# Optimization experiments

Hardware: AMD Instinct MI355X
Metric: run time of the kernel (lower is better)

The kernel has to match this reference:

```python
import jax, jax.numpy as jnp
import numpy as np

B, N, F_IN, D_OUT, EMB_DIM = 4, 2048, 64, 128, 16
H1, D1 = 4, D_OUT // 4   # gat1: 4 heads, 32 per head
H2, D2 = 1, D_OUT        # gat2: 1 head, 128
NEG_INF = -1e9
LN_EPS = 1e-3  # keras LayerNormalization default epsilon


def setup_inputs() -> dict:
    key = jax.random.key(0)
    ks = jax.random.split(key, 12)
    def glorot(k, shape):
        lim = np.sqrt(6.0 / (shape[0] + shape[1]))
        return jax.random.uniform(k, shape, jnp.float32, -lim, lim)
    return {
        "x": jax.random.normal(ks[0], (B, N, F_IN), jnp.float32),
        "emb": glorot(ks[1], (N, EMB_DIM)),
        "q1_w": glorot(ks[2], (F_IN, H1 * D1)), "q1_b": jnp.zeros((H1 * D1,), jnp.float32),
        "k1_w": glorot(ks[3], (F_IN, H1 * D1)), "k1_b": jnp.zeros((H1 * D1,), jnp.float32),
        "v1_w": glorot(ks[4], (F_IN, H1 * D1)), "v1_b": jnp.zeros((H1 * D1,), jnp.float32),
        "q2_w": glorot(ks[5], (D_OUT, H2 * D2)), "q2_b": jnp.zeros((H2 * D2,), jnp.float32),
        "k2_w": glorot(ks[6], (D_OUT, H2 * D2)), "k2_b": jnp.zeros((H2 * D2,), jnp.float32),
        "v2_w": glorot(ks[7], (D_OUT, H2 * D2)), "v2_b": jnp.zeros((H2 * D2,), jnp.float32),
        "proj_w": glorot(ks[8], (F_IN, D_OUT)),
        "ln_g": jnp.ones((D_OUT,), jnp.float32),
        "ln_b": jnp.zeros((D_OUT,), jnp.float32),
    }


def _adaptive_adj(emb):
    # tf.math.l2_normalize(axis=-1, epsilon=1e-12)
    sq = jnp.maximum(jnp.sum(emb * emb, axis=-1, keepdims=True), 1e-12)
    n = emb * jax.lax.rsqrt(sq)
    adj = jax.nn.sigmoid(n @ n.T)
    eye = jnp.eye(N, dtype=jnp.float32)
    return adj + eye - adj * eye  # force diag to 1


def _graph_attention(x, adj, qw, qb, kw, kb, vw, vb, heads, d):
    b, n, _ = x.shape
    q = (x @ qw + qb).reshape(b, n, heads, d)
    k = (x @ kw + kb).reshape(b, n, heads, d)
    v = (x @ vw + vb).reshape(b, n, heads, d)
    scores = jnp.einsum('bihd,bjhd->bhij', q, k) / jnp.sqrt(jnp.float32(d))
    scores = jnp.where(adj[None, None] == 0, NEG_INF, scores)
    w = jax.nn.softmax(scores, axis=-1)  # dropout inactive (training=False)
    out = jnp.einsum('bhij,bjhd->bihd', w, v)
    return out.reshape(b, n, heads * d)


def reference(x, emb, q1_w, q1_b, k1_w, k1_b, v1_w, v1_b,
              q2_w, q2_b, k2_w, k2_b, v2_w, v2_b, proj_w, ln_g, ln_b):
    input_projected = x @ proj_w
    adj = _adaptive_adj(emb)
    h = _graph_attention(x, adj, q1_w, q1_b, k1_w, k1_b, v1_w, v1_b, H1, D1)
    h = jax.nn.relu(h)
    h = _graph_attention(h, adj, q2_w, q2_b, k2_w, k2_b, v2_w, v2_b, H2, D2)
    y = h + input_projected
    mu = jnp.mean(y, axis=-1, keepdims=True)
    var = jnp.mean((y - mu) ** 2, axis=-1, keepdims=True)
    return (y - mu) * jax.lax.rsqrt(var + LN_EPS) * ln_g + ln_b
```

## Files before the change

### kernel.cpp

```cpp
#include <hip/hip_runtime.h>
#include <hip/hip_bf16.h>

#define NB 4
#define NN 2048
#define FIN 64
#define DOUT 128

typedef __hip_bfloat16 bf16;
typedef __attribute__((ext_vector_type(8))) short short8;
typedef __attribute__((ext_vector_type(4))) float f32x4;
typedef __attribute__((ext_vector_type(4))) int int4v;

static __device__ __forceinline__ float bf2f(bf16 v) { return __bfloat162float(v); }
static __device__ __forceinline__ bf16  f2bf(float v) { return __float2bfloat16(v); }
static __device__ __forceinline__ unsigned bfbits(float v) {
    bf16 h = __float2bfloat16(v);
    return (unsigned)*reinterpret_cast<unsigned short*>(&h);
}

#define VT_IDX(b, key, d) ((((size_t)(b)*32 + ((key) >> 6))*128 + (d))*64 + ((key) & 63))

__global__ __launch_bounds__(256) void k_gemm1(
    const float* __restrict__ x,
    const float* __restrict__ q1w, const float* __restrict__ q1b,
    const float* __restrict__ k1w, const float* __restrict__ k1b,
    const float* __restrict__ v1w, const float* __restrict__ v1b,
    const float* __restrict__ pw,
    bf16* __restrict__ qA, bf16* __restrict__ kA, bf16* __restrict__ vT,
    float* __restrict__ proj)
{
    __shared__ float At[64][65];
    __shared__ float Wt[64][65];
    const int rb = blockIdx.x;
    const int cb = blockIdx.y;
    const int mat = cb >> 1;
    const int c0 = (cb & 1) * 64;
    const float* W    = (mat==0)? q1w : (mat==1)? k1w : (mat==2)? v1w : pw;
    const float* bias = (mat==0)? q1b : (mat==1)? k1b : (mat==2)? v1b : nullptr;
    const int t = threadIdx.x;
    const int row0 = rb * 64;
    for (int e = t; e < 64*64; e += 256) {
        int r = e >> 6, c = e & 63;
        At[r][c] = x[(size_t)(row0 + r)*FIN + c];
        Wt[r][c] = W[r*DOUT + c0 + c];
    }
    __syncthreads();
    const int ty = t >> 4, tx = t & 15;
    float acc[4][4] = {};
    #pragma unroll 8
    for (int k = 0; k < 64; ++k) {
        float av[4], bv[4];
        #pragma unroll
        for (int i = 0; i < 4; ++i) av[i] = At[ty*4+i][k];
        #pragma unroll
        for (int j = 0; j < 4; ++j) bv[j] = Wt[k][tx*4+j];
        #pragma unroll
        for (int i = 0; i < 4; ++i)
            #pragma unroll
            for (int j = 0; j < 4; ++j)
                acc[i][j] = fmaf(av[i], bv[j], acc[i][j]);
    }
    #pragma unroll
    for (int i = 0; i < 4; ++i) {
        int gr = row0 + ty*4 + i;
        #pragma unroll
        for (int j = 0; j < 4; ++j) {
            int gc = c0 + tx*4 + j;
            float v = acc[i][j] + (bias ? bias[gc] : 0.f);
            if (mat == 0)      qA[(size_t)gr*DOUT + gc] = f2bf(v);
            else if (mat == 1) kA[(size_t)gr*DOUT + gc] = f2bf(v);
            else if (mat == 2) {
                int b = gr >> 11, n = gr & 2047;
                vT[VT_IDX(b, n, gc)] = f2bf(v);
            } else proj[(size_t)gr*DOUT + gc] = v;
        }
    }
}

__global__ __launch_bounds__(256) void k_gemm2(
    const bf16* __restrict__ h,
    const float* __restrict__ q2w, const float* __restrict__ q2b,
    const float* __restrict__ k2w, const float* __restrict__ k2b,
    const float* __restrict__ v2w, const float* __restrict__ v2b,
    bf16* __restrict__ qA, bf16* __restrict__ kA, bf16* __restrict__ vT)
{
    __shared__ float At[64][65];
    __shared__ float Wt[64][65];
    const int rb = blockIdx.x, cb = blockIdx.y;
    const int mat = cb >> 1, c0 = (cb & 1)*64;
    const float* W    = (mat==0)? q2w : (mat==1)? k2w : v2w;
    const float* bias = (mat==0)? q2b : (mat==1)? k2b : v2b;
    const int t = threadIdx.x, ty = t >> 4, tx = t & 15, row0 = rb*64;
    float acc[4][4] = {};
    for (int kc = 0; kc < 2; ++kc) {
        __syncthreads();
        for (int e = t; e < 64*64; e += 256) {
            int r = e >> 6, c = e & 63;
            At[r][c] = bf2f(h[(size_t)(row0+r)*DOUT + kc*64 + c]);
            Wt[r][c] = W[(kc*64+r)*DOUT + c0 + c];
        }
        __syncthreads();
        #pragma unroll 8
        for (int k = 0; k < 64; ++k) {
            float av[4], bv[4];
            #pragma unroll
            for (int i = 0; i < 4; ++i) av[i] = At[ty*4+i][k];
            #pragma unroll
            for (int j = 0; j < 4; ++j) bv[j] = Wt[k][tx*4+j];
            #pragma unroll
            for (int i = 0; i < 4; ++i)
                #pragma unroll
                for (int j = 0; j < 4; ++j)
                    acc[i][j] = fmaf(av[i], bv[j], acc[i][j]);
        }
    }
    #pragma unroll
    for (int i = 0; i < 4; ++i) {
        int gr = row0 + ty*4 + i;
        #pragma unroll
        for (int j = 0; j < 4; ++j) {
            int gc = c0 + tx*4 + j;
            float v = acc[i][j] + bias[gc];
            if (mat == 0)      qA[(size_t)gr*DOUT + gc] = f2bf(v);
            else if (mat == 1) kA[(size_t)gr*DOUT + gc] = f2bf(v);
            else {
                int b = gr >> 11, n = gr & 2047;
                vT[VT_IDX(b, n, gc)] = f2bf(v);
            }
        }
    }
}

template<int D, int MODE, int NW, int NQ>
__global__ __launch_bounds__(NW*64, 2) void k_attn_mfma(
    const bf16* __restrict__ qA, const bf16* __restrict__ kA, const bf16* __restrict__ vT,
    const float* __restrict__ proj, const float* __restrict__ lng, const float* __restrict__ lnb,
    bf16* __restrict__ hout, float* __restrict__ fout)
{
    constexpr int NKS = D / 32;
    constexpr int NMT = D / 16;
    constexpr int ITERS = NN / (64 * NW);

    __shared__ float lbuf[NW][NQ*16];
    constexpr int OSW = (MODE == 0) ? (D + 1) : (D + 2);
    __shared__ char oS_raw[(size_t)NW * NQ*16 * OSW * ((MODE == 0) ? 4 : 2)];

    const float scale = (D == 32) ? 0.17677669529663687f : 0.08838834764831843f;

    const unsigned wg  = blockIdx.x + (unsigned)gridDim.x * blockIdx.y;
    const unsigned xcd = wg & 7u;
    const unsigned idx = wg >> 3;
    int qb, bh;
    if constexpr (MODE == 0) {
        bh = (int)((xcd << 1) | (idx >> 5));
        qb = (int)(idx & 31u);
    } else {
        bh = (int)(xcd >> 1);
        qb = (int)(((xcd & 1u) << 5) | idx);
    }

    const int b  = (MODE == 0) ? (bh >> 2) : bh;
    const int hd = (MODE == 0) ? (bh & 3) : 0;
    const int q0 = qb * (16*NQ);
    const int wave = threadIdx.x >> 6, lane = threadIdx.x & 63;
    const int n16 = lane & 15, q4 = lane >> 4;

    const short* qbase = (const short*)qA + ((size_t)b*NN)*DOUT + hd*32;
    const short* kbase = (const short*)kA + ((size_t)b*NN)*DOUT + hd*32;
    const short* vbase = (const short*)vT + (size_t)b*32*128*64 + (size_t)(hd*32)*64;

    short8 qf[NQ][NKS];
    #pragma unroll
    for (int qq = 0; qq < NQ; ++qq)
        #pragma unroll
        for (int ks = 0; ks < NKS; ++ks)
            qf[qq][ks] = *(const short8*)(qbase + (size_t)(q0 + qq*16 + n16)*DOUT + ks*32 + q4*8);

    f32x4 acc[NQ][NMT];
    #pragma unroll
    for (int qq = 0; qq < NQ; ++qq)
        #pragma unroll
        for (int mt = 0; mt < NMT; ++mt) acc[qq][mt] = f32x4{0.f, 0.f, 0.f, 0.f};
    float l_lane[NQ];
    #pragma unroll
    for (int qq = 0; qq < NQ; ++qq) l_lane[qq] = 0.f;

    const int srcA = n16 + ((q4 & 1) * 2) * 16;
    const int srcB = srcA + 16;
    const bool selhi = (q4 >= 2);

    for (int kt0 = 0; kt0 < ITERS; ++kt0) {
        const int kt = wave * ITERS + kt0;
        const short* krow = kbase + (size_t)(kt*64)*DOUT;
        const short* vrow = vbase + (size_t)kt*128*64;

        unsigned w0v[NQ][4], w1v[NQ][4];
        #pragma unroll
        for (int mt = 0; mt < 4; ++mt) {
            f32x4 c[NQ];
            #pragma unroll
            for (int qq = 0; qq < NQ; ++qq) c[qq] = f32x4{0.f, 0.f, 0.f, 0.f};
            #pragma unroll
            for (int ks = 0; ks < NKS; ++ks) {
                short8 kf = *(const short8*)(krow + (size_t)(mt*16 + n16)*DOUT + ks*32 + q4*8);
                #pragma unroll
                for (int qq = 0; qq < NQ; ++qq)
                    c[qq] = __builtin_amdgcn_mfma_f32_16x16x32_bf16(kf, qf[qq][ks], c[qq], 0, 0, 0);
            }
            #pragma unroll
            for (int qq = 0; qq < NQ; ++qq) {
                #pragma unroll
                for (int r = 0; r < 4; ++r) {
                    float p = __expf(c[qq][r] * scale);
                    c[qq][r] = p;
                    l_lane[qq] += p;
                }
                w0v[qq][mt] = bfbits(c[qq][0]) | (bfbits(c[qq][1]) << 16);
                w1v[qq][mt] = bfbits(c[qq][2]) | (bfbits(c[qq][3]) << 16);
            }
        }

        #pragma unroll
        for (int ks2 = 0; ks2 < 2; ++ks2) {
            const int t0 = ks2*2, t1 = ks2*2 + 1;
            short8 pf[NQ];
            #pragma unroll
            for (int qq = 0; qq < NQ; ++qq) {
                int4v pw;
                { unsigned a = __shfl(w0v[qq][t0], srcA), bx = __shfl(w0v[qq][t1], srcA);
                  pw.x = selhi ? (int)bx : (int)a; }
                { unsigned a = __shfl(w1v[qq][t0], srcA), bx = __shfl(w1v[qq][t1], srcA);
                  pw.y = selhi ? (int)bx : (int)a; }
                { unsigned a = __shfl(w0v[qq][t0], srcB), bx = __shfl(w0v[qq][t1], srcB);
                  pw.z = selhi ? (int)bx : (int)a; }
                { unsigned a = __shfl(w1v[qq][t0], srcB), bx = __shfl(w1v[qq][t1], srcB);
                  pw.w = selhi ? (int)bx : (int)a; }
                pf[qq] = __builtin_bit_cast(short8, pw);
            }
            #pragma unroll
            for (int mt = 0; mt < NMT; ++mt) {
                short8 vf = *(const short8*)(vrow + (size_t)(mt*16 + n16)*64 + ks2*32 + q4*8);
                #pragma unroll
                for (int qq = 0; qq < NQ; ++qq)
                    acc[qq][mt] = __builtin_amdgcn_mfma_f32_16x16x32_bf16(vf, pf[qq], acc[qq][mt], 0, 0, 0);
            }
        }
    }

    #pragma unroll
    for (int qq = 0; qq < NQ; ++qq) {
        l_lane[qq] += __shfl_xor(l_lane[qq], 16);
        l_lane[qq] += __shfl_xor(l_lane[qq], 32);
        if (q4 == 0) lbuf[wave][qq*16 + n16] = l_lane[qq];
    }

    if (MODE == 0) {
        float (&oSf)[NW][NQ*16][D + 1] = *reinterpret_cast<float (*)[NW][NQ*16][D + 1]>(oS_raw);
        #pragma unroll
        for (int qq = 0; qq < NQ; ++qq)
            #pragma unroll
            for (int mt = 0; mt < NMT; ++mt)
                #pragma unroll
                for (int r = 0; r < 4; ++r)
                    oSf[wave][qq*16 + n16][mt*16 + q4*4 + r] = acc[qq][mt][r];
    } else {
        unsigned short (&oSh)[NW][NQ*16][D + 2] =
            *reinterpret_cast<unsigned short (*)[NW][NQ*16][D + 2]>(oS_raw);
        #pragma unroll
        for (int qq = 0; qq < NQ; ++qq)
            #pragma unroll
            for (int mt = 0; mt < NMT; ++mt)
                #pragma unroll
                for (int r = 0; r < 4; ++r)
                    oSh[wave][qq*16 + n16][mt*16 + q4*4 + r] = (unsigned short)bfbits(acc[qq][mt][r]);
    }
    __syncthreads();

    if (MODE == 0) {
        float (&oSf)[NW][NQ*16][D + 1] = *reinterpret_cast<float (*)[NW][NQ*16][D + 1]>(oS_raw);
        if (wave < 4) {
            const int ql = (wave & 3)*4 + (lane >> 4);
            const int d2 = (lane & 15)*2;
            #pragma unroll
            for (int qq = 0; qq < NQ; ++qq) {
                const int row = qq*16 + ql;
                float denom = 0.f, o0 = 0.f, o1 = 0.f;
                #pragma unroll
                for (int s = 0; s < NW; ++s) {
                    denom += lbuf[s][row];
                    o0 += oSf[s][row][d2];
                    o1 += oSf[s][row][d2 + 1];
                }
                float di = 1.f / denom;
                unsigned w = bfbits(fmaxf(o0*di, 0.f)) | (bfbits(fmaxf(o1*di, 0.f)) << 16);
                *(unsigned*)&hout[((size_t)b*NN + q0 + row)*DOUT + hd*32 + d2] = w;
            }
        }
    } else {
        unsigned short (&oSh)[NW][NQ*16][D + 2] =
            *reinterpret_cast<unsigned short (*)[NW][NQ*16][D + 2]>(oS_raw);
        const int ql = wave*2 + (lane >> 5);
        const int il = lane & 31;
        #pragma unroll
        for (int qq = 0; qq < NQ; ++qq) {
            const int row = qq*16 + ql;
            float denom = 0.f;
            #pragma unroll
            for (int s = 0; s < NW; ++s) denom += lbuf[s][row];
            float di = 1.f / denom;
            size_t base = ((size_t)b*NN + q0 + row)*DOUT + il*4;
            float4 pr = *(const float4*)(proj + base);
            float y[4];
            #pragma unroll
            for (int c = 0; c < 4; ++c) {
                float o = 0.f;
                #pragma unroll
                for (int s = 0; s < NW; ++s)
                    o += __uint_as_float(((unsigned)oSh[s][row][il*4 + c]) << 16);
                y[c] = o*di + ((const float*)&pr)[c];
            }
            float ssum = y[0] + y[1] + y[2] + y[3];
            #pragma unroll
            for (int off = 16; off >= 1; off >>= 1) ssum += __shfl_xor(ssum, off);
            float mu = ssum * (1.f/128.f);
            float vs = 0.f;
            #pragma unroll
            for (int c = 0; c < 4; ++c) { float d = y[c] - mu; vs += d*d; }
            #pragma unroll
            for (int off = 16; off >= 1; off >>= 1) vs += __shfl_xor(vs, off);
            float rs = rsqrtf(vs * (1.f/128.f) + 1e-3f);
            float4 g4 = *(const float4*)(lng + il*4);
            float4 b4 = *(const float4*)(lnb + il*4);
            float4 o4;
            #pragma unroll
            for (int c = 0; c < 4; ++c) {
                float o = (y[c] - mu)*rs*((const float*)&g4)[c] + ((const float*)&b4)[c];
                if (!(o == o)) o = 12345.0f;
                ((float*)&o4)[c] = o;
            }
            *(float4*)(fout + base) = o4;
        }
    }
}

extern "C" void kernel_launch(void* const* d_in, const int* in_sizes, int n_in,
                              void* d_out, int out_size, void* d_ws, size_t ws_size,
                              hipStream_t stream)
{
    const float* x   = (const float*)d_in[0];
    const float* q1w = (const float*)d_in[2];
    const float* q1b = (const float*)d_in[3];
    const float* k1w = (const float*)d_in[4];
    const float* k1b = (const float*)d_in[5];
    const float* v1w = (const float*)d_in[6];
    const float* v1b = (const float*)d_in[7];
    const float* q2w = (const float*)d_in[8];
    const float* q2b = (const float*)d_in[9];
    const float* k2w = (const float*)d_in[10];
    const float* k2b = (const float*)d_in[11];
    const float* v2w = (const float*)d_in[12];
    const float* v2b = (const float*)d_in[13];
    const float* pw  = (const float*)d_in[14];
    const float* lng = (const float*)d_in[15];
    const float* lnb = (const float*)d_in[16];

    const size_t SZ = (size_t)NB*NN*DOUT;
    char* wsb = (char*)d_ws;
    bf16*  qA   = (bf16*)(wsb + 0*SZ*2);
    bf16*  kA   = (bf16*)(wsb + 1*SZ*2);
    bf16*  vT   = (bf16*)(wsb + 2*SZ*2);
    float* proj = (float*)(wsb + 3*SZ*2);
    bf16*  h    = (bf16*)(wsb + 3*SZ*2 + SZ*4);

    k_gemm1<<<dim3(128, 8), 256, 0, stream>>>(x, q1w, q1b, k1w, k1b, v1w, v1b, pw,
                                              qA, kA, vT, proj);
    k_attn_mfma<32, 0, 8, 4><<<dim3(32, 16), 512, 0, stream>>>(
        qA, kA, vT, nullptr, nullptr, nullptr, h, nullptr);
    k_gemm2<<<dim3(128, 6), 256, 0, stream>>>(h, q2w, q2b, k2w, k2b, v2w, v2b,
                                              qA, kA, vT);
    k_attn_mfma<128, 1, 8, 2><<<dim3(64, 4), 512, 0, stream>>>(
        qA, kA, vT, proj, lng, lnb, nullptr, (float*)d_out);
}
```

Measured before the change: 195.5 us.

## Pre-swizzle Q/K/V into MFMA fragment order for contiguous wave loads

The projection GEMMs now write Q, K and V in a layout that matches the MFMA operand fragments, so each lane in the attention kernel loads a contiguous 16-byte chunk at lane*8 and a wave reads one contiguous 1 KB block. This replaces the strided row loads of the old layout. The GEMM tile loads are also vectorized to float4/short8. The cost is more scattered bf16 stores in the GEMM epilogues.

```diff
diff --git a/kernel.cpp b/kernel.cpp
--- a/kernel.cpp
+++ b/kernel.cpp
@@ -18,7 +18,6 @@
     return (unsigned)*reinterpret_cast<unsigned short*>(&h);
 }
 
-#define VT_IDX(b, key, d) ((((size_t)(b)*32 + ((key) >> 6))*128 + (d))*64 + ((key) & 63))
 
 __global__ __launch_bounds__(256) void k_gemm1(
     const float* __restrict__ x,
@@ -39,10 +38,10 @@
     const float* bias = (mat==0)? q1b : (mat==1)? k1b : (mat==2)? v1b : nullptr;
     const int t = threadIdx.x;
     const int row0 = rb * 64;
-    for (int e = t; e < 64*64; e += 256) {
-        int r = e >> 6, c = e & 63;
-        At[r][c] = x[(size_t)(row0 + r)*FIN + c];
-        Wt[r][c] = W[r*DOUT + c0 + c];
+    for (int e = t; e < 1024; e += 256) {
+        int r = e >> 4, c4 = e & 15;
+        *(float4*)&At[r][c4*4] = *(const float4*)&x[(size_t)(row0 + r)*FIN + c4*4];
+        *(float4*)&Wt[r][c4*4] = *(const float4*)&W[(size_t)r*DOUT + c0 + c4*4];
     }
     __syncthreads();
     const int ty = t >> 4, tx = t & 15;
@@ -63,16 +62,24 @@
     #pragma unroll
     for (int i = 0; i < 4; ++i) {
         int gr = row0 + ty*4 + i;
+        int b = gr >> 11, n = gr & 2047;
         #pragma unroll
         for (int j = 0; j < 4; ++j) {
             int gc = c0 + tx*4 + j;
             float v = acc[i][j] + (bias ? bias[gc] : 0.f);
-            if (mat == 0)      qA[(size_t)gr*DOUT + gc] = f2bf(v);
-            else if (mat == 1) kA[(size_t)gr*DOUT + gc] = f2bf(v);
-            else if (mat == 2) {
-                int b = gr >> 11, n = gr & 2047;
-                vT[VT_IDX(b, n, gc)] = f2bf(v);
-            } else proj[(size_t)gr*DOUT + gc] = v;
+            if (mat == 3) { proj[(size_t)gr*DOUT + gc] = v; continue; }
+            int hd = gc >> 5, d32 = gc & 31;
+            if (mat == 2) {
+                int kt = n >> 6, ks2 = (n >> 5) & 1, q4k = (n >> 3) & 3, jk = n & 7;
+                int mt = d32 >> 4, n16d = d32 & 15;
+                size_t idx = ((((size_t)(b*4+hd)*32 + kt)*2 + mt)*2 + ks2)*512
+                             + (size_t)(q4k*16 + n16d)*8 + jk;
+                vT[idx] = f2bf(v);
+            } else {
+                size_t idx = ((size_t)(b*4+hd)*128 + (n >> 4))*512
+                             + (size_t)((d32 >> 3)*16 + (n & 15))*8 + (d32 & 7);
+                if (mat == 0) qA[idx] = f2bf(v); else kA[idx] = f2bf(v);
+            }
         }
     }
 }
@@ -94,10 +101,16 @@
     float acc[4][4] = {};
     for (int kc = 0; kc < 2; ++kc) {
         __syncthreads();
-        for (int e = t; e < 64*64; e += 256) {
-            int r = e >> 6, c = e & 63;
-            At[r][c] = bf2f(h[(size_t)(row0+r)*DOUT + kc*64 + c]);
-            Wt[r][c] = W[(kc*64+r)*DOUT + c0 + c];
+        for (int e = t; e < 512; e += 256) {
+            int r = e >> 3, c8 = e & 7;
+            short8 hv = *(const short8*)&h[(size_t)(row0+r)*DOUT + kc*64 + c8*8];
+            #pragma unroll
+            for (int u = 0; u < 8; ++u)
+                At[r][c8*8 + u] = __uint_as_float(((unsigned)(unsigned short)hv[u]) << 16);
+        }
+        for (int e = t; e < 1024; e += 256) {
+            int r = e >> 4, c4 = e & 15;
+            *(float4*)&Wt[r][c4*4] = *(const float4*)&W[(size_t)(kc*64+r)*DOUT + c0 + c4*4];
         }
         __syncthreads();
         #pragma unroll 8
@@ -117,15 +130,22 @@
     #pragma unroll
     for (int i = 0; i < 4; ++i) {
         int gr = row0 + ty*4 + i;
+        int b = gr >> 11, n = gr & 2047;
         #pragma unroll
         for (int j = 0; j < 4; ++j) {
             int gc = c0 + tx*4 + j;
             float v = acc[i][j] + bias[gc];
-            if (mat == 0)      qA[(size_t)gr*DOUT + gc] = f2bf(v);
-            else if (mat == 1) kA[(size_t)gr*DOUT + gc] = f2bf(v);
-            else {
-                int b = gr >> 11, n = gr & 2047;
-                vT[VT_IDX(b, n, gc)] = f2bf(v);
+            if (mat == 2) {
+                int kt = n >> 6, ks2 = (n >> 5) & 1, q4k = (n >> 3) & 3, jk = n & 7;
+                int mt = gc >> 4, n16d = gc & 15;
+                size_t idx = (((size_t)b*32 + kt)*8 + mt)*1024 + (size_t)ks2*512
+                             + (size_t)(q4k*16 + n16d)*8 + jk;
+                vT[idx] = f2bf(v);
+            } else {
+                int ks = gc >> 5, q4 = (gc >> 3) & 3, jj = gc & 7;
+                size_t idx = ((size_t)b*128 + (n >> 4))*2048 + (size_t)ks*512
+                             + (size_t)(q4*16 + (n & 15))*8 + jj;
+                if (mat == 0) qA[idx] = f2bf(v); else kA[idx] = f2bf(v);
             }
         }
     }
@@ -164,17 +184,25 @@
     const int q0 = qb * (16*NQ);
     const int wave = threadIdx.x >> 6, lane = threadIdx.x & 63;
     const int n16 = lane & 15, q4 = lane >> 4;
-
-    const short* qbase = (const short*)qA + ((size_t)b*NN)*DOUT + hd*32;
-    const short* kbase = (const short*)kA + ((size_t)b*NN)*DOUT + hd*32;
-    const short* vbase = (const short*)vT + (size_t)b*32*128*64 + (size_t)(hd*32)*64;
+    const int lane8 = lane * 8;
+
+    const short* qbase, * kbase, * vbase;
+    if constexpr (MODE == 0) {
+        qbase = (const short*)qA + (size_t)(b*4 + hd)*128*512;
+        kbase = (const short*)kA + (size_t)(b*4 + hd)*128*512;
+        vbase = (const short*)vT + (size_t)(b*4 + hd)*(32*NMT*2*512);
+    } else {
+        qbase = (const short*)qA + (size_t)b*128*NKS*512;
+        kbase = (const short*)kA + (size_t)b*128*NKS*512;
+        vbase = (const short*)vT + (size_t)b*(32*NMT*2*512);
+    }
 
     short8 qf[NQ][NKS];
     #pragma unroll
     for (int qq = 0; qq < NQ; ++qq)
         #pragma unroll
         for (int ks = 0; ks < NKS; ++ks)
-            qf[qq][ks] = *(const short8*)(qbase + (size_t)(q0 + qq*16 + n16)*DOUT + ks*32 + q4*8);
+            qf[qq][ks] = *(const short8*)(qbase + ((size_t)(qb*NQ + qq)*NKS + ks)*512 + lane8);
 
     f32x4 acc[NQ][NMT];
     #pragma unroll
@@ -191,8 +219,6 @@
 
     for (int kt0 = 0; kt0 < ITERS; ++kt0) {
         const int kt = wave * ITERS + kt0;
-        const short* krow = kbase + (size_t)(kt*64)*DOUT;
-        const short* vrow = vbase + (size_t)kt*128*64;
 
         unsigned w0v[NQ][4], w1v[NQ][4];
         #pragma unroll
@@ -202,7 +228,7 @@
             for (int qq = 0; qq < NQ; ++qq) c[qq] = f32x4{0.f, 0.f, 0.f, 0.f};
             #pragma unroll
             for (int ks = 0; ks < NKS; ++ks) {
-                short8 kf = *(const short8*)(krow + (size_t)(mt*16 + n16)*DOUT + ks*32 + q4*8);
+                short8 kf = *(const short8*)(kbase + ((size_t)(kt*4 + mt)*NKS + ks)*512 + lane8);
                 #pragma unroll
                 for (int qq = 0; qq < NQ; ++qq)
                     c[qq] = __builtin_amdgcn_mfma_f32_16x16x32_bf16(kf, qf[qq][ks], c[qq], 0, 0, 0);
@@ -239,7 +265,7 @@
             }
             #pragma unroll
             for (int mt = 0; mt < NMT; ++mt) {
-                short8 vf = *(const short8*)(vrow + (size_t)(mt*16 + n16)*64 + ks2*32 + q4*8);
+                short8 vf = *(const short8*)(vbase + (((size_t)kt*NMT + mt)*2 + ks2)*512 + lane8);
                 #pragma unroll
                 for (int qq = 0; qq < NQ; ++qq)
                     acc[qq][mt] = __builtin_amdgcn_mfma_f32_16x16x32_bf16(vf, pf[qq], acc[qq][mt], 0, 0, 0);
```

New measurement: 190.2 us. 1.03x faster.
